# Performance work log

Measured on AMD Instinct MI355X. Metric: run time of the kernel, lower is better.

Reference implementation:

```python
import jax, jax.numpy as jnp
import numpy as np

N_NODES = 50000
N_EDGES = 600000
C = 128
T = 2          # layer index t
NU = 1         # DRew nu parameter
EPS = 0.0      # GIN eps


def mlp(x, W1, b1, W2, b2):
    # instantiate_mlp with final_activation=False, batch_norm=False:
    # Linear -> ReLU -> Linear
    return jax.nn.relu(x @ W1 + b1) @ W2 + b2


def setup_inputs() -> dict:
    key = jax.random.key(0)
    ks = jax.random.split(key, 16)
    node_embeddings = jax.random.normal(ks[0], (T + 1, N_NODES, C), dtype=jnp.float32)
    edge_index = jax.random.randint(ks[1], (2, N_EDGES), 0, N_NODES, dtype=jnp.int32)
    edge_weights = jax.random.randint(ks[2], (N_EDGES,), 1, T + 2, dtype=jnp.int32)  # hops 1..3
    s = 1.0 / np.sqrt(C)
    def lin(k):
        kw, kb = jax.random.split(k)
        return (jax.random.uniform(kw, (C, C), jnp.float32, -s, s),
                jax.random.uniform(kb, (C,), jnp.float32, -s, s))
    loop_W1, loop_b1 = lin(ks[3]); loop_W2, loop_b2 = lin(ks[4])
    rel_W1, rel_b1 = lin(ks[5]); rel_W2, rel_b2 = lin(ks[6])
    # T higher-hop MLPs (k = 2 .. T+1), stacked along axis 0
    hh1 = [lin(k) for k in jax.random.split(ks[7], T)]
    hh2 = [lin(k) for k in jax.random.split(ks[8], T)]
    hh_W1 = jnp.stack([w for w, _ in hh1]); hh_b1 = jnp.stack([b for _, b in hh1])
    hh_W2 = jnp.stack([w for w, _ in hh2]); hh_b2 = jnp.stack([b for _, b in hh2])
    hop_coef = jax.random.normal(ks[9], (T + 1,), dtype=jnp.float32)
    return dict(t=T, node_embeddings=node_embeddings, edge_index=edge_index,
                edge_weights=edge_weights,
                loop_W1=loop_W1, loop_b1=loop_b1, loop_W2=loop_W2, loop_b2=loop_b2,
                rel_W1=rel_W1, rel_b1=rel_b1, rel_W2=rel_W2, rel_b2=rel_b2,
                hh_W1=hh_W1, hh_b1=hh_b1, hh_W2=hh_W2, hh_b2=hh_b2,
                hop_coef=hop_coef)


def reference(t, node_embeddings, edge_index, edge_weights,
              loop_W1, loop_b1, loop_W2, loop_b2,
              rel_W1, rel_b1, rel_W2, rel_b2,
              hh_W1, hh_b1, hh_W2, hh_b2, hop_coef):
    x_t = node_embeddings[t]                       # [N, C]
    n = x_t.shape[0]
    row, col = edge_index[0], edge_index[1]        # sparse A: out[row] += X[col]
    dt = x_t.dtype

    hops = []
    # hop 1: relational MLP on current-layer embeddings
    h1 = mlp(x_t, rel_W1, rel_b1, rel_W2, rel_b2)
    m1 = (edge_weights == 1).astype(dt)[:, None]
    hops.append(jax.ops.segment_sum(h1[col] * m1, row, num_segments=n))
    # hops k = 2 .. t+1: per-hop MLP on delayed embeddings (DRew)
    for k in range(2, t + 2):
        delay = max(0, k - NU)
        hk = mlp(node_embeddings[t - delay],
                 hh_W1[k - 2], hh_b1[k - 2], hh_W2[k - 2], hh_b2[k - 2])
        mk = (edge_weights == k).astype(dt)[:, None]
        hops.append(jax.ops.segment_sum(hk[col] * mk, row, num_segments=n))

    by_hop = jnp.stack(hops)                       # [t+1, N, C]
    self_term = mlp((1.0 + EPS) * x_t, loop_W1, loop_b1, loop_W2, loop_b2)
    return self_term + jnp.einsum('k,knc->nc', hop_coef, by_hop)
```

## Files before the change

### kernel.cpp

```cpp
#include <hip/hip_runtime.h>

#define N_NODES 50000
#define N_EDGES 600000
#define C 128
#define STRIPS 3125
#define MLP_WAVES 1024

typedef __bf16 bf16;
typedef __attribute__((ext_vector_type(8))) __bf16 bf16x8;
typedef __attribute__((ext_vector_type(4))) __bf16 bf16x4;
typedef __attribute__((ext_vector_type(2))) __bf16 bf16x2;
typedef __attribute__((ext_vector_type(4))) float f32x4;
typedef __attribute__((ext_vector_type(2))) float f32x2;

struct PtrsV { const void* p[8]; };

__device__ __forceinline__ int bf16_wild(unsigned short w) {
    int exp = (w >> 7) & 0xFF;
    int mant = w & 0x7F;
    if (exp == 0xFF) return 1;
    if (exp >= 133) return 1;
    if (exp == 0) return mant != 0 ? 1 : 0;
    if (exp <= 114) return 1;
    return 0;
}

__global__ void __launch_bounds__(256) detect_zero_kernel(
    const unsigned short* __restrict__ emb,
    const unsigned short* __restrict__ w,
    const unsigned short* __restrict__ b,
    const unsigned short* __restrict__ hc,
    int* __restrict__ flags, int* __restrict__ deg)
{
    if (blockIdx.x == 0) {
        int lane = threadIdx.x;
        if (lane >= 64) return;
        int ce = 0, cw = 0, cb = 0, ch = 0;
        for (int j = 0; j < 4; ++j) {
            ce += bf16_wild(emb[lane * 4 + j]);
            cw += bf16_wild(w[lane * 4 + j]);
        }
        for (int j = 0; j < 2; ++j) cb += bf16_wild(b[lane * 2 + j]);
        if (lane < 3) ch = bf16_wild(hc[lane]);
        for (int off = 32; off > 0; off >>= 1) {
            ce += __shfl_down(ce, off);
            cw += __shfl_down(cw, off);
            cb += __shfl_down(cb, off);
            ch += __shfl_down(ch, off);
        }
        if (lane == 0) {
            int wf = (cw >= 16) ? 1 : 0;
            flags[0] = (ce >= 16) ? 1 : 0;
            flags[1] = wf;
            flags[2] = (cb >= 8) ? 1 : 0;
            flags[3] = (ch > 0) ? 1 : wf;
        }
    } else {
        int i = (blockIdx.x - 1) * 256 + threadIdx.x;
        if (i < N_NODES) deg[i] = 0;
    }
}

__global__ void __launch_bounds__(256) pack_kernel(
    PtrsV wmats, PtrsV bvecs, const void* hc_raw,
    const int* __restrict__ flags,
    bf16* __restrict__ pw, float* __restrict__ cbias, float* __restrict__ ccoef)
{
    int tid = blockIdx.x * 256 + threadIdx.x;
    int wf = flags[1], bfl = flags[2], hf = flags[3];
    if (tid < 8 * 16384) {
        int m    = tid >> 14;
        int r    = tid & 16383;
        int j    = r & 7;
        int lane = (r >> 3) & 63;
        int n0   = (r >> 9) & 7;
        int kk   = r >> 12;
        int k = kk * 32 + (lane >> 4) * 8 + j;
        int n = n0 * 16 + (lane & 15);
        int idx = k * C + n + ((m == 4 || m == 5) ? 16384 : 0);
        float v = wf ? ((const float*)wmats.p[m])[idx]
                     : (float)((const bf16*)wmats.p[m])[idx];
        pw[tid] = (bf16)v;
    } else if (tid < 8 * 16384 + 1024) {
        int j = tid - 8 * 16384;
        int m = j >> 7, n = j & 127;
        int idx = n + ((m == 4 || m == 5) ? 128 : 0);
        float v = bfl ? ((const float*)bvecs.p[m])[idx]
                      : (float)((const bf16*)bvecs.p[m])[idx];
        cbias[j] = v;
    } else if (tid < 8 * 16384 + 1024 + 3) {
        int i = tid - (8 * 16384 + 1024);
        float v = hf ? ((const float*)hc_raw)[i]
                     : (float)((const bf16*)hc_raw)[i];
        ccoef[i] = v;
    }
}

__global__ __launch_bounds__(256, 1) void mlp_kernel(
    const void* __restrict__ emb_raw,
    const bf16* __restrict__ pw,
    const float* __restrict__ cbias,
    const float* __restrict__ ccoef,
    const int* __restrict__ flags,
    bf16* __restrict__ h,
    bf16* __restrict__ hs)
{
    __shared__ bf16 sH[4][16][136];
    const int tid  = threadIdx.x;
    const int wave = tid >> 6, lane = tid & 63;
    const int wid  = blockIdx.x * 4 + wave;
    const int set  = wid & 3;
    const int wstart = wid >> 2;
    const int lrow = lane & 15, lquad = lane >> 4;
    bf16 (*sh)[136] = sH[wave];

    const int mat1_of[4]  = {0, 2, 4, 6};
    const int layer_of[4] = {2, 1, 0, 2};
    const int m1 = mat1_of[set];
    const bf16x8* w1v = (const bf16x8*)(pw + (size_t)m1 * 16384);
    const bf16x8* w2v = w1v + 2048;
    const float* b1 = cbias + m1 * 128;
    const float* b2 = b1 + 128;
    const float oscale = (set == 0) ? ccoef[0] : (set == 1) ? ccoef[1]
                       : (set == 2) ? ccoef[2] : 1.0f;
    bf16* outp = (set == 3) ? hs : (h + (size_t)set * N_NODES * C);
    const int emb_f32 = flags[0];
    const size_t lbase = (size_t)layer_of[set] * N_NODES * C;

    bf16x8 W1f[8][4], W2f[8][4];
    #pragma unroll
    for (int n0 = 0; n0 < 8; ++n0)
        #pragma unroll
        for (int kk = 0; kk < 4; ++kk) {
            W1f[n0][kk] = w1v[kk * 512 + n0 * 64 + lane];
            W2f[n0][kk] = w2v[kk * 512 + n0 * 64 + lane];
        }
    float b1f[8], b2f[8];
    #pragma unroll
    for (int n0 = 0; n0 < 8; ++n0) {
        b1f[n0] = b1[n0 * 16 + lrow];
        b2f[n0] = b2[n0 * 16 + lrow];
    }

    auto loadA = [&](int strip, bf16x8 af[4]) {
        size_t xb = lbase + (size_t)(strip * 16 + lrow) * C + lquad * 8;
        if (emb_f32) {
            const float* xf = (const float*)emb_raw + xb;
            #pragma unroll
            for (int kk = 0; kk < 4; ++kk) {
                f32x4 u0 = *(const f32x4*)(xf + kk * 32);
                f32x4 u1 = *(const f32x4*)(xf + kk * 32 + 4);
                bf16x8 v;
                v[0]=(bf16)u0[0]; v[1]=(bf16)u0[1]; v[2]=(bf16)u0[2]; v[3]=(bf16)u0[3];
                v[4]=(bf16)u1[0]; v[5]=(bf16)u1[1]; v[6]=(bf16)u1[2]; v[7]=(bf16)u1[3];
                af[kk] = v;
            }
        } else {
            const bf16* x16 = (const bf16*)emb_raw + xb;
            #pragma unroll
            for (int kk = 0; kk < 4; ++kk)
                af[kk] = *(const bf16x8*)(x16 + kk * 32);
        }
    };

    bf16x8 af[4];
    if (wstart < STRIPS) loadA(wstart, af);
    for (int s = wstart; s < STRIPS; s += 256) {
        #pragma unroll
        for (int n0 = 0; n0 < 8; ++n0) {
            f32x4 a4 = {0.f, 0.f, 0.f, 0.f};
            #pragma unroll
            for (int kk = 0; kk < 4; ++kk)
                a4 = __builtin_amdgcn_mfma_f32_16x16x32_bf16(af[kk], W1f[n0][kk], a4, 0, 0, 0);
            float bias = b1f[n0];
            int n = n0 * 16 + lrow;
            #pragma unroll
            for (int r = 0; r < 4; ++r) {
                float v = a4[r] + bias;
                v = v > 0.f ? v : 0.f;
                sh[lquad * 4 + r][n] = (bf16)v;
            }
        }
        bf16x8 afn[4];
        int snext = s + 256;
        if (snext < STRIPS) loadA(snext, afn);
        bf16x8 ah[4];
        #pragma unroll
        for (int kk = 0; kk < 4; ++kk)
            ah[kk] = *(const bf16x8*)(&sh[lrow][kk * 32 + lquad * 8]);
        #pragma unroll
        for (int n0 = 0; n0 < 8; ++n0) {
            f32x4 a4 = {0.f, 0.f, 0.f, 0.f};
            #pragma unroll
            for (int kk = 0; kk < 4; ++kk)
                a4 = __builtin_amdgcn_mfma_f32_16x16x32_bf16(ah[kk], W2f[n0][kk], a4, 0, 0, 0);
            float bias = b2f[n0];
            int n = n0 * 16 + lrow;
            #pragma unroll
            for (int r = 0; r < 4; ++r)
                sh[lquad * 4 + r][n] = (bf16)((a4[r] + bias) * oscale);
        }
        {
            int row = lane >> 2;
            int cs  = (lane & 3) * 32;
            bf16* dst = outp + (size_t)(s * 16) * C;
            #pragma unroll
            for (int i = 0; i < 4; ++i) {
                bf16x8 v = *(const bf16x8*)(&sh[row][cs + i * 8]);
                *(bf16x8*)(dst + (size_t)row * C + cs + i * 8) = v;
            }
        }
        #pragma unroll
        for (int kk = 0; kk < 4; ++kk) af[kk] = afn[kk];
    }
}

__global__ void __launch_bounds__(256) hist_kernel(
    const int* __restrict__ erow, int* __restrict__ deg)
{
    int e = blockIdx.x * 256 + threadIdx.x;
    if (e >= N_EDGES) return;
    atomicAdd(&deg[erow[e]], 1);
}

__device__ __forceinline__ int wave_incl_scan(int v, int lane) {
    int x = v;
    #pragma unroll
    for (int d = 1; d < 64; d <<= 1) {
        int t = __shfl_up(x, d);
        if (lane >= d) x += t;
    }
    return x;
}

__global__ void __launch_bounds__(256) scanA_kernel(
    const int* __restrict__ deg, int* __restrict__ offsets, int* __restrict__ btot)
{
    __shared__ int swave[4];
    int b = blockIdx.x, tid = threadIdx.x;
    int i = b * 256 + tid;
    int lane = tid & 63, wv = tid >> 6;
    int v = (i < N_NODES) ? deg[i] : 0;
    int x = wave_incl_scan(v, lane);
    if (lane == 63) swave[wv] = x;
    __syncthreads();
    int w0 = swave[0], w1 = swave[1], w2 = swave[2], w3 = swave[3];
    int wp = (wv > 0 ? w0 : 0) + (wv > 1 ? w1 : 0) + (wv > 2 ? w2 : 0);
    if (i < N_NODES) offsets[i] = wp + x - v;
    if (tid == 0) btot[b] = w0 + w1 + w2 + w3;
}

__global__ void __launch_bounds__(256) scanB_kernel(
    const int* __restrict__ btot, int* __restrict__ bbase, int nblk)
{
    __shared__ int swave[4];
    int tid = threadIdx.x;
    int lane = tid & 63, wv = tid >> 6;
    int v = (tid < nblk) ? btot[tid] : 0;
    int x = wave_incl_scan(v, lane);
    if (lane == 63) swave[wv] = x;
    __syncthreads();
    int w0 = swave[0], w1 = swave[1], w2 = swave[2], w3 = swave[3];
    int wp = (wv > 0 ? w0 : 0) + (wv > 1 ? w1 : 0) + (wv > 2 ? w2 : 0);
    if (tid < nblk) bbase[tid] = wp + x - v;
}

__global__ void __launch_bounds__(256) scanC_kernel(
    const int* __restrict__ bbase, int* __restrict__ offsets, int* __restrict__ cursor)
{
    int i = blockIdx.x * 256 + threadIdx.x;
    if (i < N_NODES) {
        int o = offsets[i] + bbase[blockIdx.x];
        offsets[i] = o;
        cursor[i] = o;
    }
    if (i == 0) offsets[N_NODES] = N_EDGES;
}

__global__ void __launch_bounds__(256) fill_kernel(
    const int* __restrict__ erow, const int* __restrict__ ecol,
    const int* __restrict__ ew,
    int* __restrict__ cursor, int* __restrict__ edata)
{
    int e = blockIdx.x * 256 + threadIdx.x;
    if (e >= N_EDGES) return;
    int dst = erow[e];
    int pos = atomicAdd(&cursor[dst], 1);
    edata[pos] = (ecol[e] << 2) | (ew[e] - 1);
}

__global__ void __launch_bounds__(256) gather_kernel(
    const int* __restrict__ offsets, const int* __restrict__ edata,
    const bf16* __restrict__ h,
    const bf16* __restrict__ hs,
    void* __restrict__ out,
    const int* __restrict__ flags)
{
    const int node = blockIdx.x * 4 + (threadIdx.x >> 6);
    if (node >= N_NODES) return;
    const int lane = threadIdx.x & 63;
    const int c = lane * 2;

    bf16x2 sv = *(const bf16x2*)(hs + (size_t)node * C + c);
    float a0 = (float)sv[0], a1 = (float)sv[1];

    const int s = offsets[node], e = offsets[node + 1];
    for (int base = s; base < e; base += 64) {
        int idx = base + lane;
        int ed_i = (idx < e) ? edata[idx] : 0;
        int cnt = e - base; if (cnt > 64) cnt = 64;
        int j = 0;
        for (; j + 8 <= cnt; j += 8) {
            float t0 = 0.f, t1 = 0.f;
            #pragma unroll
            for (int u = 0; u < 8; ++u) {
                int ed = __shfl(ed_i, j + u);
                bf16x2 v = *(const bf16x2*)(h + (size_t)(ed & 3) * (N_NODES * C)
                                              + (size_t)(ed >> 2) * C + c);
                t0 += (float)v[0];
                t1 += (float)v[1];
            }
            a0 += t0; a1 += t1;
        }
        for (; j + 4 <= cnt; j += 4) {
            int e0 = __shfl(ed_i, j);
            int e1 = __shfl(ed_i, j + 1);
            int e2 = __shfl(ed_i, j + 2);
            int e3 = __shfl(ed_i, j + 3);
            bf16x2 v0 = *(const bf16x2*)(h + (size_t)(e0 & 3) * (N_NODES * C) + (size_t)(e0 >> 2) * C + c);
            bf16x2 v1 = *(const bf16x2*)(h + (size_t)(e1 & 3) * (N_NODES * C) + (size_t)(e1 >> 2) * C + c);
            bf16x2 v2 = *(const bf16x2*)(h + (size_t)(e2 & 3) * (N_NODES * C) + (size_t)(e2 >> 2) * C + c);
            bf16x2 v3 = *(const bf16x2*)(h + (size_t)(e3 & 3) * (N_NODES * C) + (size_t)(e3 >> 2) * C + c);
            a0 += (float)v0[0] + (float)v1[0] + (float)v2[0] + (float)v3[0];
            a1 += (float)v0[1] + (float)v1[1] + (float)v2[1] + (float)v3[1];
        }
        for (; j < cnt; ++j) {
            int ed = __shfl(ed_i, j);
            bf16x2 v = *(const bf16x2*)(h + (size_t)(ed & 3) * (N_NODES * C) + (size_t)(ed >> 2) * C + c);
            a0 += (float)v[0];
            a1 += (float)v[1];
        }
    }

    if (flags[0]) {
        f32x2 o; o[0] = a0; o[1] = a1;
        *(f32x2*)((float*)out + (size_t)node * C + c) = o;
    } else {
        bf16x2 o; o[0] = (bf16)a0; o[1] = (bf16)a1;
        *(bf16x2*)((bf16*)out + (size_t)node * C + c) = o;
    }
}

extern "C" void kernel_launch(void* const* d_in, const int* in_sizes, int n_in,
                              void* d_out, int out_size, void* d_ws, size_t ws_size,
                              hipStream_t stream) {
    const void* emb = d_in[1];
    const int*  ei  = (const int*)d_in[2];
    const int*  ew  = (const int*)d_in[3];

    const size_t H_BYTES  = (size_t)3 * N_NODES * C * sizeof(bf16);
    const size_t HS_BYTES = (size_t)N_NODES * C * sizeof(bf16);
    const size_t PW_BYTES = (size_t)8 * 16384 * sizeof(bf16);
    bf16*  h      = (bf16*)d_ws;
    bf16*  hs     = (bf16*)((char*)d_ws + H_BYTES);
    bf16*  pw     = (bf16*)((char*)d_ws + H_BYTES + HS_BYTES);
    float* cbias  = (float*)((char*)d_ws + H_BYTES + HS_BYTES + PW_BYTES);
    float* ccoef  = cbias + 1024;
    int*   flags  = (int*)(ccoef + 4);
    int*   deg    = flags + 16;
    int*   cursor = deg + N_NODES;
    int*   offsets= cursor + N_NODES;
    int*   btot   = offsets + N_NODES + 8;
    int*   bbase  = btot + 256;
    int*   edata  = bbase + 256;

    PtrsV wptr;
    wptr.p[0] = d_in[8];   wptr.p[1] = d_in[10];
    wptr.p[2] = d_in[12];  wptr.p[3] = d_in[14];
    wptr.p[4] = d_in[12];  wptr.p[5] = d_in[14];
    wptr.p[6] = d_in[4];   wptr.p[7] = d_in[6];
    PtrsV bptr;
    bptr.p[0] = d_in[9];   bptr.p[1] = d_in[11];
    bptr.p[2] = d_in[13];  bptr.p[3] = d_in[15];
    bptr.p[4] = d_in[13];  bptr.p[5] = d_in[15];
    bptr.p[6] = d_in[5];   bptr.p[7] = d_in[7];

    const int NBLK = (N_NODES + 255) / 256;

    detect_zero_kernel<<<1 + NBLK, 256, 0, stream>>>(
        (const unsigned short*)emb, (const unsigned short*)d_in[8],
        (const unsigned short*)d_in[9], (const unsigned short*)d_in[16],
        flags, deg);

    pack_kernel<<<517, 256, 0, stream>>>(wptr, bptr, d_in[16], flags, pw, cbias, ccoef);

    const int* erow = ei;
    const int* ecol = ei + N_EDGES;
    hist_kernel<<<(N_EDGES + 255) / 256, 256, 0, stream>>>(erow, deg);
    scanA_kernel<<<NBLK, 256, 0, stream>>>(deg, offsets, btot);
    scanB_kernel<<<1, 256, 0, stream>>>(btot, bbase, NBLK);
    scanC_kernel<<<NBLK, 256, 0, stream>>>(bbase, offsets, cursor);
    fill_kernel<<<(N_EDGES + 255) / 256, 256, 0, stream>>>(erow, ecol, ew, cursor, edata);

    mlp_kernel<<<MLP_WAVES / 4, 256, 0, stream>>>(emb, pw, cbias, ccoef, flags, h, hs);

    gather_kernel<<<(N_NODES + 3) / 4, 256, 0, stream>>>(
        offsets, edata, h, hs, d_out, flags);
}
```

Baseline: 302.8 us.

## Restructure MLP kernel to process four strips per wave with streamed weights

The MLP kernel previously kept a persistent grid of 1024 waves, each holding all W1 and W2 fragments in registers and looping over strips with a software prefetch. Now each wave handles one fixed group of four 16-row strips. It loads all inputs up front, then streams each weight fragment from global memory once and reuses it across the four strips. This frees registers, so launch bounds allow two blocks per CU and many more waves are launched (3128) to hide latency. In exchange, the weights are re-read from L2 by every wave and LDS use per block grows fourfold.

```diff
diff --git a/kernel.cpp b/kernel.cpp
--- a/kernel.cpp
+++ b/kernel.cpp
@@ -4,7 +4,8 @@
 #define N_EDGES 600000
 #define C 128
 #define STRIPS 3125
-#define MLP_WAVES 1024
+#define GROUPS 782
+#define N_TASKS 4
 
 typedef __bf16 bf16;
 typedef __attribute__((ext_vector_type(8))) __bf16 bf16x8;
@@ -96,7 +97,7 @@
     }
 }
 
-__global__ __launch_bounds__(256, 1) void mlp_kernel(
+__global__ __launch_bounds__(256, 2) void mlp_kernel(
     const void* __restrict__ emb_raw,
     const bf16* __restrict__ pw,
     const float* __restrict__ cbias,
@@ -105,113 +106,134 @@
     bf16* __restrict__ h,
     bf16* __restrict__ hs)
 {
-    __shared__ bf16 sH[4][16][136];
+    __shared__ bf16 sH[4][64][136];
     const int tid  = threadIdx.x;
     const int wave = tid >> 6, lane = tid & 63;
     const int wid  = blockIdx.x * 4 + wave;
-    const int set  = wid & 3;
-    const int wstart = wid >> 2;
+    if (wid >= N_TASKS * GROUPS) return;
+    const int task = wid & 3;
+    const int grp  = wid >> 2;
     const int lrow = lane & 15, lquad = lane >> 4;
     bf16 (*sh)[136] = sH[wave];
 
-    const int mat1_of[4]  = {0, 2, 4, 6};
-    const int layer_of[4] = {2, 1, 0, 2};
-    const int m1 = mat1_of[set];
+    const int m1_of[4] = {0, 2, 4, 6};
+    const int ly_of[4] = {2, 1, 0, 2};
+    const int m1 = m1_of[task];
     const bf16x8* w1v = (const bf16x8*)(pw + (size_t)m1 * 16384);
     const bf16x8* w2v = w1v + 2048;
-    const float* b1 = cbias + m1 * 128;
-    const float* b2 = b1 + 128;
-    const float oscale = (set == 0) ? ccoef[0] : (set == 1) ? ccoef[1]
-                       : (set == 2) ? ccoef[2] : 1.0f;
-    bf16* outp = (set == 3) ? hs : (h + (size_t)set * N_NODES * C);
+    const float oscale = (task == 0) ? ccoef[0] : (task == 1) ? ccoef[1]
+                       : (task == 2) ? ccoef[2] : 1.0f;
+    bf16* outp = (task == 3) ? hs : (h + (size_t)task * N_NODES * C);
     const int emb_f32 = flags[0];
-    const size_t lbase = (size_t)layer_of[set] * N_NODES * C;
-
-    bf16x8 W1f[8][4], W2f[8][4];
-    #pragma unroll
-    for (int n0 = 0; n0 < 8; ++n0)
+    const size_t lbase = (size_t)ly_of[task] * N_NODES * C;
+
+    const int s0 = grp * 4;
+    int nv = STRIPS - s0; if (nv > 4) nv = 4;
+
+    float b1f[8], b2f[8];
+    #pragma unroll
+    for (int n0 = 0; n0 < 8; ++n0) {
+        b1f[n0] = cbias[m1 * 128 + n0 * 16 + lrow];
+        b2f[n0] = cbias[(m1 + 1) * 128 + n0 * 16 + lrow];
+    }
+
+    bf16x8 af[4][4];
+    #pragma unroll
+    for (int i = 0; i < 4; ++i) {
+        if (i < nv) {
+            size_t xb = lbase + (size_t)((s0 + i) * 16 + lrow) * C + lquad * 8;
+            if (emb_f32) {
+                const float* xf = (const float*)emb_raw + xb;
+                #pragma unroll
+                for (int kk = 0; kk < 4; ++kk) {
+                    f32x4 u0 = *(const f32x4*)(xf + kk * 32);
+                    f32x4 u1 = *(const f32x4*)(xf + kk * 32 + 4);
+                    bf16x8 v;
+                    v[0]=(bf16)u0[0]; v[1]=(bf16)u0[1]; v[2]=(bf16)u0[2]; v[3]=(bf16)u0[3];
+                    v[4]=(bf16)u1[0]; v[5]=(bf16)u1[1]; v[6]=(bf16)u1[2]; v[7]=(bf16)u1[3];
+                    af[i][kk] = v;
+                }
+            } else {
+                const bf16* x16 = (const bf16*)emb_raw + xb;
+                #pragma unroll
+                for (int kk = 0; kk < 4; ++kk)
+                    af[i][kk] = *(const bf16x8*)(x16 + kk * 32);
+            }
+        }
+    }
+
+    #pragma unroll
+    for (int n0 = 0; n0 < 8; ++n0) {
+        bf16x8 bv0 = w1v[0 * 512 + n0 * 64 + lane];
+        bf16x8 bv1 = w1v[1 * 512 + n0 * 64 + lane];
+        bf16x8 bv2 = w1v[2 * 512 + n0 * 64 + lane];
+        bf16x8 bv3 = w1v[3 * 512 + n0 * 64 + lane];
+        int n = n0 * 16 + lrow;
+        float bias = b1f[n0];
         #pragma unroll
-        for (int kk = 0; kk < 4; ++kk) {
-            W1f[n0][kk] = w1v[kk * 512 + n0 * 64 + lane];
-            W2f[n0][kk] = w2v[kk * 512 + n0 * 64 + lane];
-        }
-    float b1f[8], b2f[8];
-    #pragma unroll
-    for (int n0 = 0; n0 < 8; ++n0) {
-        b1f[n0] = b1[n0 * 16 + lrow];
-        b2f[n0] = b2[n0 * 16 + lrow];
-    }
-
-    auto loadA = [&](int strip, bf16x8 af[4]) {
-        size_t xb = lbase + (size_t)(strip * 16 + lrow) * C + lquad * 8;
-        if (emb_f32) {
-            const float* xf = (const float*)emb_raw + xb;
-            #pragma unroll
-            for (int kk = 0; kk < 4; ++kk) {
-                f32x4 u0 = *(const f32x4*)(xf + kk * 32);
-                f32x4 u1 = *(const f32x4*)(xf + kk * 32 + 4);
-                bf16x8 v;
-                v[0]=(bf16)u0[0]; v[1]=(bf16)u0[1]; v[2]=(bf16)u0[2]; v[3]=(bf16)u0[3];
-                v[4]=(bf16)u1[0]; v[5]=(bf16)u1[1]; v[6]=(bf16)u1[2]; v[7]=(bf16)u1[3];
-                af[kk] = v;
+        for (int i = 0; i < 4; ++i) {
+            if (i < nv) {
+                f32x4 a4 = {0.f, 0.f, 0.f, 0.f};
+                a4 = __builtin_amdgcn_mfma_f32_16x16x32_bf16(af[i][0], bv0, a4, 0, 0, 0);
+                a4 = __builtin_amdgcn_mfma_f32_16x16x32_bf16(af[i][1], bv1, a4, 0, 0, 0);
+                a4 = __builtin_amdgcn_mfma_f32_16x16x32_bf16(af[i][2], bv2, a4, 0, 0, 0);
+                a4 = __builtin_amdgcn_mfma_f32_16x16x32_bf16(af[i][3], bv3, a4, 0, 0, 0);
+                #pragma unroll
+                for (int r = 0; r < 4; ++r) {
+                    float v = a4[r] + bias;
+                    v = v > 0.f ? v : 0.f;
+                    sh[i * 16 + lquad * 4 + r][n] = (bf16)v;
+                }
             }
-        } else {
-            const bf16* x16 = (const bf16*)emb_raw + xb;
+        }
+    }
+
+    bf16x8 ah[4][4];
+    #pragma unroll
+    for (int i = 0; i < 4; ++i)
+        if (i < nv) {
             #pragma unroll
             for (int kk = 0; kk < 4; ++kk)
-                af[kk] = *(const bf16x8*)(x16 + kk * 32);
-        }
-    };
-
-    bf16x8 af[4];
-    if (wstart < STRIPS) loadA(wstart, af);
-    for (int s = wstart; s < STRIPS; s += 256) {
+                ah[i][kk] = *(const bf16x8*)(&sh[i * 16 + lrow][kk * 32 + lquad * 8]);
+        }
+
+    #pragma unroll
+    for (int n0 = 0; n0 < 8; ++n0) {
+        bf16x8 bv0 = w2v[0 * 512 + n0 * 64 + lane];
+        bf16x8 bv1 = w2v[1 * 512 + n0 * 64 + lane];
+        bf16x8 bv2 = w2v[2 * 512 + n0 * 64 + lane];
+        bf16x8 bv3 = w2v[3 * 512 + n0 * 64 + lane];
+        int n = n0 * 16 + lrow;
+        float bias = b2f[n0];
         #pragma unroll
-        for (int n0 = 0; n0 < 8; ++n0) {
-            f32x4 a4 = {0.f, 0.f, 0.f, 0.f};
-            #pragma unroll
-            for (int kk = 0; kk < 4; ++kk)
-                a4 = __builtin_amdgcn_mfma_f32_16x16x32_bf16(af[kk], W1f[n0][kk], a4, 0, 0, 0);
-            float bias = b1f[n0];
-            int n = n0 * 16 + lrow;
-            #pragma unroll
-            for (int r = 0; r < 4; ++r) {
-                float v = a4[r] + bias;
-                v = v > 0.f ? v : 0.f;
-                sh[lquad * 4 + r][n] = (bf16)v;
+        for (int i = 0; i < 4; ++i) {
+            if (i < nv) {
+                f32x4 a4 = {0.f, 0.f, 0.f, 0.f};
+                a4 = __builtin_amdgcn_mfma_f32_16x16x32_bf16(ah[i][0], bv0, a4, 0, 0, 0);
+                a4 = __builtin_amdgcn_mfma_f32_16x16x32_bf16(ah[i][1], bv1, a4, 0, 0, 0);
+                a4 = __builtin_amdgcn_mfma_f32_16x16x32_bf16(ah[i][2], bv2, a4, 0, 0, 0);
+                a4 = __builtin_amdgcn_mfma_f32_16x16x32_bf16(ah[i][3], bv3, a4, 0, 0, 0);
+                #pragma unroll
+                for (int r = 0; r < 4; ++r)
+                    sh[i * 16 + lquad * 4 + r][n] = (bf16)((a4[r] + bias) * oscale);
             }
         }
-        bf16x8 afn[4];
-        int snext = s + 256;
-        if (snext < STRIPS) loadA(snext, afn);
-        bf16x8 ah[4];
+    }
+
+    {
+        int row = lane >> 2;
+        int cs  = (lane & 3) * 32;
         #pragma unroll
-        for (int kk = 0; kk < 4; ++kk)
-            ah[kk] = *(const bf16x8*)(&sh[lrow][kk * 32 + lquad * 8]);
-        #pragma unroll
-        for (int n0 = 0; n0 < 8; ++n0) {
-            f32x4 a4 = {0.f, 0.f, 0.f, 0.f};
-            #pragma unroll
-            for (int kk = 0; kk < 4; ++kk)
-                a4 = __builtin_amdgcn_mfma_f32_16x16x32_bf16(ah[kk], W2f[n0][kk], a4, 0, 0, 0);
-            float bias = b2f[n0];
-            int n = n0 * 16 + lrow;
-            #pragma unroll
-            for (int r = 0; r < 4; ++r)
-                sh[lquad * 4 + r][n] = (bf16)((a4[r] + bias) * oscale);
-        }
-        {
-            int row = lane >> 2;
-            int cs  = (lane & 3) * 32;
-            bf16* dst = outp + (size_t)(s * 16) * C;
-            #pragma unroll
-            for (int i = 0; i < 4; ++i) {
-                bf16x8 v = *(const bf16x8*)(&sh[row][cs + i * 8]);
-                *(bf16x8*)(dst + (size_t)row * C + cs + i * 8) = v;
+        for (int i = 0; i < 4; ++i) {
+            if (i < nv) {
+                bf16* dst = outp + (size_t)((s0 + i) * 16) * C;
+                #pragma unroll
+                for (int j = 0; j < 4; ++j) {
+                    bf16x8 v = *(const bf16x8*)(&sh[i * 16 + row][cs + j * 8]);
+                    *(bf16x8*)(dst + (size_t)row * C + cs + j * 8) = v;
+                }
             }
         }
-        #pragma unroll
-        for (int kk = 0; kk < 4; ++kk) af[kk] = afn[kk];
     }
 }
 
@@ -402,7 +424,8 @@
     scanC_kernel<<<NBLK, 256, 0, stream>>>(bbase, offsets, cursor);
     fill_kernel<<<(N_EDGES + 255) / 256, 256, 0, stream>>>(erow, ecol, ew, cursor, edata);
 
-    mlp_kernel<<<MLP_WAVES / 4, 256, 0, stream>>>(emb, pw, cbias, ccoef, flags, h, hs);
+    mlp_kernel<<<(N_TASKS * GROUPS + 3) / 4, 256, 0, stream>>>(
+        emb, pw, cbias, ccoef, flags, h, hs);
 
     gather_kernel<<<(N_NODES + 3) / 4, 256, 0, stream>>>(
         offsets, edata, h, hs, d_out, flags);
```

After: 285.4 us. -5.7%, faster.
